# Optimization experiments

Measured on AMD Instinct MI355X. Metric: run time of the kernel, lower is better.

Reference implementation:

```python
import jax, jax.numpy as jnp
import numpy as np
from jax import lax

N, C_IN, L, K, C_OUT, PAD = 16, 64, 8192, 3, 64, 1

def setup_inputs() -> dict:
    key = jax.random.key(0)
    k1, k2, k3 = jax.random.split(key, 3)
    x = jax.random.normal(k1, (N, C_IN, L), dtype=jnp.float32)
    # kaiming normal (relu): std = sqrt(2 / fan_in), fan_in = C_in * kernel_size
    std_off = np.sqrt(2.0 / (C_IN * K)).astype(np.float32)
    w_off = jax.random.normal(k2, (2 * K, C_IN, K), dtype=jnp.float32) * std_off
    b_off = jnp.zeros((2 * K,), dtype=jnp.float32)
    # 1x1 conv: fan_in = C_in * K (kernel_size 1)
    std_w = np.sqrt(2.0 / (C_IN * K)).astype(np.float32)
    w = jax.random.normal(k3, (C_OUT, C_IN * K), dtype=jnp.float32) * std_w
    b = jnp.zeros((C_OUT,), dtype=jnp.float32)
    return {"x": x, "w_off": w_off, "b_off": b_off, "w": w, "b": b}

def reference(x, w_off, b_off, w, b):
    n, c, l = x.shape
    # offset conv: Conv1d(C, 2K, K, stride=1, padding=PAD)
    offsets = lax.conv_general_dilated(
        x, w_off, window_strides=(1,), padding=[(PAD, PAD)],
        dimension_numbers=("NCH", "OIH", "NCH")) + b_off[None, :, None]
    l_out = offsets.shape[2]
    # [N, 2K, L] -> [N, K, 2, L] -> [N, L, K, 2]; only component 0 is used
    off = offsets.reshape(n, K, 2, l_out).transpose(0, 3, 1, 2)[..., 0]  # [N, L, K]
    x_pad = jnp.pad(x, ((0, 0), (0, 0), (PAD, PAD)))
    lp = l + 2 * PAD
    base = jnp.arange(PAD, lp - PAD, dtype=x.dtype)[None, :, None]  # [1, L, 1]
    grid = jnp.clip(base + off, 0.0, lp - 1)                        # [N, L, K]
    left = jnp.floor(grid).astype(jnp.int32)
    right = jnp.minimum(left + 1, lp - 1)
    alpha = grid - left.astype(x.dtype)                              # [N, L, K]
    idx_l = left.reshape(n, -1)
    idx_r = right.reshape(n, -1)
    gather = jax.vmap(lambda xp, i: xp[:, i])  # per-sample gather over length axis
    x_left = gather(x_pad, idx_l).reshape(n, c, l_out, K)
    x_right = gather(x_pad, idx_r).reshape(n, c, l_out, K)
    a = alpha[:, None]  # [N, 1, L, K]
    x_deform = (1.0 - a) * x_left + a * x_right                      # [N, C, L, K]
    # replicate torch's permute(0,3,2,1).view(N, C*K, L) exactly (row-major)
    x_deform = x_deform.transpose(0, 3, 2, 1).reshape(n, c * K, l_out)
    out = jnp.einsum("om,nml->nol", w, x_deform) + b[None, :, None]
    return out
```

## Files before the change

### kernel.cpp

```cpp
#include <hip/hip_runtime.h>
#include <hip/hip_bf16.h>
#include <math.h>

#define NB   16
#define CIN  64
#define LEN  8192
#define LP2  8195
#define COUT 64
#define MSZ  192

typedef float    f32x4  __attribute__((ext_vector_type(4)));
typedef float    f32x4u __attribute__((ext_vector_type(4), aligned(4)));
typedef _Float16 f16x8  __attribute__((ext_vector_type(8)));
typedef _Float16 f16x2  __attribute__((ext_vector_type(2)));

static __device__ inline unsigned int pkrtz(float lo, float hi) {
    return __builtin_bit_cast(unsigned int, __builtin_amdgcn_cvt_pkrtz(lo, hi));
}

__global__ __launch_bounds__(256) void prep5_kernel(
    const float* __restrict__ x, const float* __restrict__ w_off,
    const float* __restrict__ b_off, const float* __restrict__ w,
    float* __restrict__ gbuf, unsigned int* __restrict__ xt32,
    unsigned short* __restrict__ wtf)
{
    int bid = blockIdx.x;
    int tid = threadIdx.x;

    if (bid >= NB * 128) {
        int b = bid - NB * 128;
        int ot = b / 6, ks = b - ot * 6;
        #pragma unroll
        for (int h = 0; h < 2; ++h) {
            int t2 = tid + h * 256;
            int lq = t2 >> 3, s = t2 & 7;
            int o = ot * 16 + (lq & 15);
            int m = ks * 32 + (lq >> 4) * 8 + s;
            _Float16 hv = (_Float16)w[o * MSZ + m];
            wtf[b * 512 + t2] = __builtin_bit_cast(unsigned short, hv);
        }
        return;
    }

    __shared__ float ps[4][3][64];
    __shared__ unsigned int bt[64 * 33];

    int lane = tid & 63;
    int wid  = __builtin_amdgcn_readfirstlane(tid >> 6);
    int xcd = bid & 7;
    int tt  = bid >> 3;
    int n   = (xcd << 1) | (tt >> 7);
    int t   = tt & 127;
    int l0 = t << 6;
    int l  = l0 + lane;
    const float* xn = x + (size_t)n * (CIN * LEN);

    float a0 = 0.f, a1 = 0.f, a2 = 0.f;
    unsigned int pk[8];

    if (t != 0 && t != 127) {
        #pragma unroll
        for (int ci = 0; ci < 16; ci += 2) {
            int c0 = (wid << 4) | ci;
            const float* xc0 = xn + (size_t)c0 * LEN;
            const float* xc1 = xc0 + LEN;
            f32x4u v0 = *(const f32x4u*)&xc0[l - 1];
            f32x4u v1 = *(const f32x4u*)&xc1[l - 1];
            const float* wa = w_off + (size_t)c0 * 3;
            const float* wb = wa + 384;
            const float* wc = wa + 768;
            a0 = fmaf(wa[0], v0.x, a0); a0 = fmaf(wa[1], v0.y, a0); a0 = fmaf(wa[2], v0.z, a0);
            a0 = fmaf(wa[3], v1.x, a0); a0 = fmaf(wa[4], v1.y, a0); a0 = fmaf(wa[5], v1.z, a0);
            a1 = fmaf(wb[0], v0.x, a1); a1 = fmaf(wb[1], v0.y, a1); a1 = fmaf(wb[2], v0.z, a1);
            a1 = fmaf(wb[3], v1.x, a1); a1 = fmaf(wb[4], v1.y, a1); a1 = fmaf(wb[5], v1.z, a1);
            a2 = fmaf(wc[0], v0.x, a2); a2 = fmaf(wc[1], v0.y, a2); a2 = fmaf(wc[2], v0.z, a2);
            a2 = fmaf(wc[3], v1.x, a2); a2 = fmaf(wc[4], v1.y, a2); a2 = fmaf(wc[5], v1.z, a2);
            pk[ci >> 1] = pkrtz(v0.y, v1.y);
        }
    } else {
        bool okm = (l >= 1);
        bool okp = (l < LEN - 1);
        #pragma unroll
        for (int ci = 0; ci < 16; ci += 2) {
            int c0 = (wid << 4) | ci;
            const float* xc0 = xn + (size_t)c0 * LEN;
            const float* xc1 = xc0 + LEN;
            float xm0 = okm ? xc0[l - 1] : 0.f;
            float x00 = xc0[l];
            float xp0 = okp ? xc0[l + 1] : 0.f;
            float xm1 = okm ? xc1[l - 1] : 0.f;
            float x01 = xc1[l];
            float xp1 = okp ? xc1[l + 1] : 0.f;
            const float* wa = w_off + (size_t)c0 * 3;
            const float* wb = wa + 384;
            const float* wc = wa + 768;
            a0 = fmaf(wa[0], xm0, a0); a0 = fmaf(wa[1], x00, a0); a0 = fmaf(wa[2], xp0, a0);
            a0 = fmaf(wa[3], xm1, a0); a0 = fmaf(wa[4], x01, a0); a0 = fmaf(wa[5], xp1, a0);
            a1 = fmaf(wb[0], xm0, a1); a1 = fmaf(wb[1], x00, a1); a1 = fmaf(wb[2], xp0, a1);
            a1 = fmaf(wb[3], xm1, a1); a1 = fmaf(wb[4], x01, a1); a1 = fmaf(wb[5], xp1, a1);
            a2 = fmaf(wc[0], xm0, a2); a2 = fmaf(wc[1], x00, a2); a2 = fmaf(wc[2], xp0, a2);
            a2 = fmaf(wc[3], xm1, a2); a2 = fmaf(wc[4], x01, a2); a2 = fmaf(wc[5], xp1, a2);
            pk[ci >> 1] = pkrtz(x00, x01);
        }
    }

    ps[wid][0][lane] = a0;
    ps[wid][1][lane] = a1;
    ps[wid][2][lane] = a2;
    #pragma unroll
    for (int j = 0; j < 8; ++j)
        bt[lane * 33 + (wid << 3) + j] = pk[j];
    __syncthreads();

    if (tid < 192) {
        int k = tid >> 6, ll = tid & 63;
        float s = b_off[2 * k];
        #pragma unroll
        for (int w4 = 0; w4 < 4; ++w4) s += ps[w4][k][ll];
        float g = fminf(fmaxf((float)(l0 + ll + 1) + s, 0.f), 8193.f);
        gbuf[((size_t)n * LEN + l0 + ll) * 3 + k] = g;
    }

    {
        int row = tid >> 2, grp = tid & 3;
        const unsigned int* src = &bt[row * 33 + (grp << 3)];
        uint4 u0, u1;
        u0.x = src[0]; u0.y = src[1]; u0.z = src[2]; u0.w = src[3];
        u1.x = src[4]; u1.y = src[5]; u1.z = src[6]; u1.w = src[7];
        size_t base = ((size_t)n * LP2 + 1 + l0 + row) * 32 + (grp << 3);
        *(uint4*)&xt32[base]     = u0;
        *(uint4*)&xt32[base + 4] = u1;
    }
    if (t == 0   && tid < 32) xt32[((size_t)n * LP2) * 32 + tid] = 0u;
    if (t == 127 && tid < 64) xt32[((size_t)n * LP2 + 8193 + (tid >> 5)) * 32 + (tid & 31)] = 0u;
}

__global__ __launch_bounds__(256) void dconv8_kernel(
    const unsigned short* __restrict__ xt16, const unsigned short* __restrict__ wtf,
    const float* __restrict__ bias, const float* __restrict__ gbuf,
    float* __restrict__ out)
{
    __shared__ unsigned short Bl[MSZ * 64];
    __shared__ __align__(16) int2 meta[MSZ];
    int tid = threadIdx.x;

    int wg  = blockIdx.x;
    int xcd = wg & 7;
    int tt  = wg >> 3;
    int n   = (xcd << 1) | (tt >> 7);
    int p   = tt & 127;

    if (tid < MSZ) {
        int k = tid >> 6, r = tid & 63;
        int l = (r << 7) | p;
        float g  = gbuf[((size_t)n * LEN + l) * 3 + k];
        float fl = floorf(g);
        meta[tid] = make_int2((int)fl, __float_as_int(g - fl));
    }
    __syncthreads();

    const unsigned short* xb = xt16 + (size_t)n * LP2 * 64;

    #pragma unroll
    for (int j = 0; j < 6; ++j) {
        int task = tid + (j << 8);
        int m  = task >> 3;
        int ch = task & 7;
        int2 mv = meta[m];
        float a = __int_as_float(mv.y);
        _Float16 ah = (_Float16)a;
        f16x2 a2; a2[0] = ah; a2[1] = ah;
        const unsigned short* rl = xb + ((size_t)(unsigned)mv.x << 6) + (ch << 3);
        uint4 vl4 = *(const uint4*)rl;
        uint4 vr4 = *(const uint4*)(rl + 64);
        const f16x2* vlh = (const f16x2*)&vl4;
        const f16x2* vrh = (const f16x2*)&vr4;
        uint4 ov;
        unsigned int* ovp = (unsigned int*)&ov;
        #pragma unroll
        for (int q = 0; q < 4; ++q) {
            f16x2 r = vlh[q] + a2 * (vrh[q] - vlh[q]);
            ovp[q] = __builtin_bit_cast(unsigned int, r);
        }
        int dst = (m << 6) + ((ch << 3) ^ (((m >> 3) & 3) << 4));
        *(uint4*)&Bl[dst] = ov;
    }
    __syncthreads();

    int lane = tid & 63;
    int ct   = tid >> 6;
    int g4   = lane >> 4;
    int c    = (ct << 4) | (lane & 15);

    f32x4 acc[4] = {};

    #pragma unroll
    for (int ks = 0; ks < 6; ++ks) {
        int mb = ks * 32 + (g4 << 3);
        int cx = c ^ ((((unsigned)(mb >> 3)) & 3) << 4);
        f16x8 afrag;
        #pragma unroll
        for (int s = 0; s < 8; ++s)
            afrag[s] = __builtin_bit_cast(_Float16, Bl[((mb + s) << 6) + cx]);

        #pragma unroll
        for (int ot = 0; ot < 4; ++ot) {
            f16x8 bfrag = *(const f16x8*)(wtf + ((size_t)(((ot * 6 + ks) << 6) + lane) << 3));
            acc[ot] = __builtin_amdgcn_mfma_f32_16x16x32_f16(afrag, bfrag, acc[ot], 0, 0, 0);
        }
    }

    int q0 = (p << 6) + ct * 16 + g4 * 4;
    #pragma unroll
    for (int ot = 0; ot < 4; ++ot) {
        int o = ot * 16 + (lane & 15);
        float bb = bias[o];
        float4 r4;
        r4.x = acc[ot][0] + bb;
        r4.y = acc[ot][1] + bb;
        r4.z = acc[ot][2] + bb;
        r4.w = acc[ot][3] + bb;
        *(float4*)&out[((size_t)n * COUT + o) * LEN + q0] = r4;
    }
}

extern "C" void kernel_launch(void* const* d_in, const int* in_sizes, int n_in,
                              void* d_out, int out_size, void* d_ws, size_t ws_size,
                              hipStream_t stream) {
    const float* x     = (const float*)d_in[0];
    const float* w_off = (const float*)d_in[1];
    const float* b_off = (const float*)d_in[2];
    const float* w     = (const float*)d_in[3];
    const float* b     = (const float*)d_in[4];
    float* out = (float*)d_out;

    const size_t GBUF_B = (size_t)NB * LEN * 3 * sizeof(float);
    const size_t WTF_B  = (size_t)MSZ * COUT * sizeof(short);
    float*          gbuf = (float*)d_ws;
    unsigned short* wtf  = (unsigned short*)((char*)d_ws + GBUF_B);
    unsigned int*   xt32 = (unsigned int*)((char*)d_ws + GBUF_B + WTF_B);
    unsigned short* xt16 = (unsigned short*)xt32;

    prep5_kernel<<<NB * 128 + 24, 256, 0, stream>>>(x, w_off, b_off, w, gbuf, xt32, wtf);
    dconv8_kernel<<<NB * 128, 256, 0, stream>>>(xt16, wtf, b, gbuf, out);
}
```

Baseline: 33.54 us.

## Process two tiles per workgroup, overlapping second gather with first MFMA

Each workgroup of the deformable-conv kernel now handles two positions (p0, p1) instead of one, halving the grid to 1024 blocks. The gather loads for the second tile are issued before the MFMA phase of the first, so global-memory latency can hide behind matrix math. The per-block meta shared-array stage is removed and gbuf is read directly in the gather. The trade-off is higher register pressure from holding 12 uint4 plus 6 alphas in flight, and fewer blocks, which may lower occupancy and parallelism.

After: 33.85 us. Within noise of the previous version (+0.9%).

```diff
diff --git a/kernel.cpp b/kernel.cpp
--- a/kernel.cpp
+++ b/kernel.cpp
@@ -135,93 +135,120 @@
     if (t == 127 && tid < 64) xt32[((size_t)n * LP2 + 8193 + (tid >> 5)) * 32 + (tid & 31)] = 0u;
 }
 
-__global__ __launch_bounds__(256) void dconv8_kernel(
+__global__ __launch_bounds__(256) void dconv11_kernel(
     const unsigned short* __restrict__ xt16, const unsigned short* __restrict__ wtf,
     const float* __restrict__ bias, const float* __restrict__ gbuf,
     float* __restrict__ out)
 {
     __shared__ unsigned short Bl[MSZ * 64];
-    __shared__ __align__(16) int2 meta[MSZ];
     int tid = threadIdx.x;
 
     int wg  = blockIdx.x;
     int xcd = wg & 7;
     int tt  = wg >> 3;
-    int n   = (xcd << 1) | (tt >> 7);
-    int p   = tt & 127;
-
-    if (tid < MSZ) {
-        int k = tid >> 6, r = tid & 63;
-        int l = (r << 7) | p;
-        float g  = gbuf[((size_t)n * LEN + l) * 3 + k];
-        float fl = floorf(g);
-        meta[tid] = make_int2((int)fl, __float_as_int(g - fl));
-    }
-    __syncthreads();
+    int n   = (xcd << 1) | (tt >> 6);
+    int pp  = tt & 63;
+    int p0  = pp << 1, p1 = p0 | 1;
 
     const unsigned short* xb = xt16 + (size_t)n * LP2 * 64;
-
-    #pragma unroll
-    for (int j = 0; j < 6; ++j) {
-        int task = tid + (j << 8);
-        int m  = task >> 3;
-        int ch = task & 7;
-        int2 mv = meta[m];
-        float a = __int_as_float(mv.y);
-        _Float16 ah = (_Float16)a;
-        f16x2 a2; a2[0] = ah; a2[1] = ah;
-        const unsigned short* rl = xb + ((size_t)(unsigned)mv.x << 6) + (ch << 3);
-        uint4 vl4 = *(const uint4*)rl;
-        uint4 vr4 = *(const uint4*)(rl + 64);
-        const f16x2* vlh = (const f16x2*)&vl4;
-        const f16x2* vrh = (const f16x2*)&vr4;
-        uint4 ov;
-        unsigned int* ovp = (unsigned int*)&ov;
-        #pragma unroll
-        for (int q = 0; q < 4; ++q) {
-            f16x2 r = vlh[q] + a2 * (vrh[q] - vlh[q]);
-            ovp[q] = __builtin_bit_cast(unsigned int, r);
-        }
-        int dst = (m << 6) + ((ch << 3) ^ (((m >> 3) & 3) << 4));
-        *(uint4*)&Bl[dst] = ov;
-    }
-    __syncthreads();
+    const float* gb = gbuf + (size_t)n * (LEN * 3);
+
+    #define GATHER(P, VL, VR, AL) do {                                        \
+        _Pragma("unroll")                                                     \
+        for (int j = 0; j < 6; ++j) {                                         \
+            int task = tid + (j << 8);                                        \
+            int m  = task >> 3;                                               \
+            int ch = task & 7;                                                \
+            int k = m >> 6, r = m & 63;                                       \
+            int l = (r << 7) | (P);                                           \
+            float g  = gb[l * 3 + k];                                         \
+            float fl = floorf(g);                                             \
+            (AL)[j] = g - fl;                                                 \
+            const unsigned short* rl = xb + ((size_t)(unsigned)(int)fl << 6) + (ch << 3); \
+            (VL)[j] = *(const uint4*)rl;                                      \
+            (VR)[j] = *(const uint4*)(rl + 64);                               \
+        }                                                                     \
+    } while (0)
+
+    #define LERPWRITE(VL, VR, AL) do {                                        \
+        _Pragma("unroll")                                                     \
+        for (int j = 0; j < 6; ++j) {                                         \
+            int task = tid + (j << 8);                                        \
+            int m  = task >> 3;                                               \
+            int ch = task & 7;                                                \
+            _Float16 ah = (_Float16)(AL)[j];                                  \
+            f16x2 a2v; a2v[0] = ah; a2v[1] = ah;                              \
+            const f16x2* vlh = (const f16x2*)&(VL)[j];                        \
+            const f16x2* vrh = (const f16x2*)&(VR)[j];                        \
+            uint4 ov;                                                         \
+            unsigned int* ovp = (unsigned int*)&ov;                           \
+            _Pragma("unroll")                                                 \
+            for (int q = 0; q < 4; ++q) {                                     \
+                f16x2 rr = vlh[q] + a2v * (vrh[q] - vlh[q]);                  \
+                ovp[q] = __builtin_bit_cast(unsigned int, rr);                \
+            }                                                                 \
+            int dst = (m << 6) + ((ch << 3) ^ (((m >> 3) & 3) << 4));         \
+            *(uint4*)&Bl[dst] = ov;                                           \
+        }                                                                     \
+    } while (0)
 
     int lane = tid & 63;
     int ct   = tid >> 6;
     int g4   = lane >> 4;
     int c    = (ct << 4) | (lane & 15);
 
-    f32x4 acc[4] = {};
-
-    #pragma unroll
-    for (int ks = 0; ks < 6; ++ks) {
-        int mb = ks * 32 + (g4 << 3);
-        int cx = c ^ ((((unsigned)(mb >> 3)) & 3) << 4);
-        f16x8 afrag;
-        #pragma unroll
-        for (int s = 0; s < 8; ++s)
-            afrag[s] = __builtin_bit_cast(_Float16, Bl[((mb + s) << 6) + cx]);
-
-        #pragma unroll
-        for (int ot = 0; ot < 4; ++ot) {
-            f16x8 bfrag = *(const f16x8*)(wtf + ((size_t)(((ot * 6 + ks) << 6) + lane) << 3));
-            acc[ot] = __builtin_amdgcn_mfma_f32_16x16x32_f16(afrag, bfrag, acc[ot], 0, 0, 0);
-        }
-    }
-
-    int q0 = (p << 6) + ct * 16 + g4 * 4;
-    #pragma unroll
-    for (int ot = 0; ot < 4; ++ot) {
-        int o = ot * 16 + (lane & 15);
-        float bb = bias[o];
-        float4 r4;
-        r4.x = acc[ot][0] + bb;
-        r4.y = acc[ot][1] + bb;
-        r4.z = acc[ot][2] + bb;
-        r4.w = acc[ot][3] + bb;
-        *(float4*)&out[((size_t)n * COUT + o) * LEN + q0] = r4;
-    }
+    #define MFMA_STORE(P) do {                                                \
+        f32x4 acc[4] = {};                                                    \
+        _Pragma("unroll")                                                     \
+        for (int ks = 0; ks < 6; ++ks) {                                      \
+            int mb = ks * 32 + (g4 << 3);                                     \
+            int cx = c ^ ((((unsigned)(mb >> 3)) & 3) << 4);                  \
+            f16x8 afrag;                                                      \
+            _Pragma("unroll")                                                 \
+            for (int s = 0; s < 8; ++s)                                       \
+                afrag[s] = __builtin_bit_cast(_Float16, Bl[((mb + s) << 6) + cx]); \
+            _Pragma("unroll")                                                 \
+            for (int ot = 0; ot < 4; ++ot) {                                  \
+                f16x8 bfrag = *(const f16x8*)(wtf + ((size_t)(((ot * 6 + ks) << 6) + lane) << 3)); \
+                acc[ot] = __builtin_amdgcn_mfma_f32_16x16x32_f16(afrag, bfrag, acc[ot], 0, 0, 0); \
+            }                                                                 \
+        }                                                                     \
+        int q0 = ((P) << 6) + ct * 16 + g4 * 4;                               \
+        _Pragma("unroll")                                                     \
+        for (int ot = 0; ot < 4; ++ot) {                                      \
+            int o = ot * 16 + (lane & 15);                                    \
+            float bb = bias[o];                                               \
+            float4 r4;                                                        \
+            r4.x = acc[ot][0] + bb;                                           \
+            r4.y = acc[ot][1] + bb;                                           \
+            r4.z = acc[ot][2] + bb;                                           \
+            r4.w = acc[ot][3] + bb;                                           \
+            *(float4*)&out[((size_t)n * COUT + o) * LEN + q0] = r4;           \
+        }                                                                     \
+    } while (0)
+
+    uint4 vlA[6], vrA[6];
+    float alA[6];
+    uint4 vlB[6], vrB[6];
+    float alB[6];
+
+    GATHER(p0, vlA, vrA, alA);
+    LERPWRITE(vlA, vrA, alA);
+    __syncthreads();
+
+    GATHER(p1, vlB, vrB, alB);
+
+    MFMA_STORE(p0);
+    __syncthreads();
+
+    LERPWRITE(vlB, vrB, alB);
+    __syncthreads();
+
+    MFMA_STORE(p1);
+
+    #undef GATHER
+    #undef LERPWRITE
+    #undef MFMA_STORE
 }
 
 extern "C" void kernel_launch(void* const* d_in, const int* in_sizes, int n_in,
@@ -242,5 +269,5 @@
     unsigned short* xt16 = (unsigned short*)xt32;
 
     prep5_kernel<<<NB * 128 + 24, 256, 0, stream>>>(x, w_off, b_off, w, gbuf, xt32, wtf);
-    dconv8_kernel<<<NB * 128, 256, 0, stream>>>(xt16, wtf, b, gbuf, out);
-}
+    dconv11_kernel<<<NB * 64, 256, 0, stream>>>(xt16, wtf, b, gbuf, out);
+}
```
